# Optimization experiments

Measured on AMD Instinct MI355X. Metric: run time of the kernel, lower is better.

## Reference

```python
import jax, jax.numpy as jnp
import numpy as np

EPS = 1e-5  # torch BatchNorm2d default


def _conv1x1(x, w):
    # x: [n, cin, h, w], w: [cout, cin] (1x1 conv == per-pixel matmul)
    return jnp.einsum('nchw,oc->nohw', x, w)


def _bn(x, gamma, beta, mean, var):
    # inference-mode BatchNorm2d over channel dim
    scale = gamma * jax.lax.rsqrt(var + EPS)
    shift = beta - mean * scale
    return x * scale[None, :, None, None] + shift[None, :, None, None]


def setup_inputs() -> dict:
    key = jax.random.key(0)
    ks = jax.random.split(key, 24)
    n, c, h, w = 16, 256, 64, 64
    width, planes = c // 2, c
    inp = {
        'x': jax.random.normal(ks[0], (n, c, h, w), jnp.float32),
        'w_theta': jax.random.normal(ks[1], (width, c), jnp.float32) * 0.05,
        'w_phi': jax.random.normal(ks[2], (width, c), jnp.float32) * 0.05,
        'w_g': jax.random.normal(ks[3], (width, c), jnp.float32) * 0.05,
        'w_zeta': jax.random.normal(ks[4], (planes, width), jnp.float32) * 0.05,
    }
    for i, (name, dim) in enumerate([('bn1', width), ('bn2', width), ('bn3', width), ('bn4', planes)]):
        k = 5 + 4 * i
        inp[f'{name}_gamma'] = jax.random.uniform(ks[k], (dim,), jnp.float32, 0.5, 1.5)
        inp[f'{name}_beta'] = jax.random.normal(ks[k + 1], (dim,), jnp.float32) * 0.1
        inp[f'{name}_mean'] = jax.random.normal(ks[k + 2], (dim,), jnp.float32) * 0.1
        inp[f'{name}_var'] = jax.random.uniform(ks[k + 3], (dim,), jnp.float32, 0.5, 1.5)
    return inp


def reference(x, w_theta, w_phi, w_g, w_zeta,
              bn1_gamma, bn1_beta, bn1_mean, bn1_var,
              bn2_gamma, bn2_beta, bn2_mean, bn2_var,
              bn3_gamma, bn3_beta, bn3_mean, bn3_var,
              bn4_gamma, bn4_beta, bn4_mean, bn4_var):
    n, c, h, w = x.shape
    theta = jax.nn.relu(_bn(_conv1x1(x, w_theta), bn1_gamma, bn1_beta, bn1_mean, bn1_var))
    phi = jax.nn.relu(_bn(_conv1x1(x, w_phi), bn2_gamma, bn2_beta, bn2_mean, bn2_var))
    g = jax.nn.relu(_bn(_conv1x1(x, w_g), bn3_gamma, bn3_beta, bn3_mean, bn3_var))

    width = theta.shape[1]
    hw = h * w
    theta = theta.reshape(n, width, hw)  # [n, C', S]
    phi = phi.reshape(n, width, hw)      # [n, C', S]
    g = g.reshape(n, width, hw)          # [n, C', S]

    # (theta^T @ phi) @ g^T == theta^T @ (phi @ g^T): no softmax, so associativity
    # lets us contract over pixels first -> O(S*C'^2) instead of O(S^2*C').
    kv = jnp.einsum('ncs,nds->ncd', phi, g)      # [n, C', C']
    out = jnp.einsum('ncs,ncd->nsd', theta, kv)  # [n, S, C']

    # faithful to torch: reshape (not transpose) [n, S, C'] -> [n, C', h, w]
    out = out.reshape(n, width, h, w)
    out = _bn(_conv1x1(out, w_zeta), bn4_gamma, bn4_beta, bn4_mean, bn4_var)
    return jax.nn.relu(out + x)
```

## Files before the change

kernel.cpp:

```cpp
#include <hip/hip_runtime.h>

#define BN_EPS 1e-5f

typedef unsigned short u16;
typedef __bf16 bf16x8 __attribute__((ext_vector_type(8)));
typedef float floatx4 __attribute__((ext_vector_type(4)));
typedef u16 u16x4 __attribute__((ext_vector_type(4)));
typedef u16 u16x8 __attribute__((ext_vector_type(8)));

__device__ __forceinline__ u16 f2bf(float f) {
    union { float f; unsigned int u; } v; v.f = f;
    unsigned int r = (v.u + 0x7fffu + ((v.u >> 16) & 1u)) >> 16;
    return (u16)r;
}

__device__ __forceinline__ void gld16(const void* gsrc, void* ldst) {
    __builtin_amdgcn_global_load_lds(
        (const __attribute__((address_space(1))) unsigned int*)gsrc,
        (__attribute__((address_space(3))) unsigned int*)ldst, 16, 0, 0);
}

__device__ __forceinline__ int addsw(int seg, int s) {
    return (seg + (s & 7) + ((s >> 3) & 7)) & 7;
}

__global__ __launch_bounds__(256) void prep_kernel(
    const float* __restrict__ wt, const float* __restrict__ wp,
    const float* __restrict__ wg, const float* __restrict__ wz,
    const float* __restrict__ g1, const float* __restrict__ b1,
    const float* __restrict__ m1, const float* __restrict__ v1,
    const float* __restrict__ g2, const float* __restrict__ b2,
    const float* __restrict__ m2, const float* __restrict__ v2,
    const float* __restrict__ g3, const float* __restrict__ b3,
    const float* __restrict__ m3, const float* __restrict__ v3,
    const float* __restrict__ g4, const float* __restrict__ b4,
    const float* __restrict__ m4, const float* __restrict__ v4,
    u16* __restrict__ W1bf, float* __restrict__ shift1,
    u16* __restrict__ Wzbf, float* __restrict__ shift4)
{
    int id = blockIdx.x * 256 + threadIdx.x;
    if (id < 384 * 256) {
        int r = id >> 8, c = id & 255;
        int grp = r >> 7, ch = r & 127;
        const float* wsrc = grp == 0 ? wt : (grp == 1 ? wp : wg);
        const float* gg = grp == 0 ? g1 : (grp == 1 ? g2 : g3);
        const float* bb = grp == 0 ? b1 : (grp == 1 ? b2 : b3);
        const float* mm = grp == 0 ? m1 : (grp == 1 ? m2 : m3);
        const float* vv = grp == 0 ? v1 : (grp == 1 ? v2 : v3);
        float scale = gg[ch] * rsqrtf(vv[ch] + BN_EPS);
        W1bf[id] = f2bf(wsrc[ch * 256 + c] * scale);
        if (c == 0) shift1[r] = bb[ch] - mm[ch] * scale;
    }
    if (id < 256 * 128) {
        int o = id >> 7;
        float scale = g4[o] * rsqrtf(v4[o] + BN_EPS);
        Wzbf[id] = f2bf(wz[id] * scale);
        if ((id & 127) == 0) shift4[o] = b4[o] - m4[o] * scale;
    }
}

__global__ __launch_bounds__(256) void gemm1_kernel(
    const float* __restrict__ x, const u16* __restrict__ W1,
    const float* __restrict__ shift1,
    u16* __restrict__ theta_sm, u16* __restrict__ pg)
{
    const int st = blockIdx.x, mt = blockIdx.y, n = blockIdx.z;
    const int tid = threadIdx.x;
    const int w = tid >> 6, lane = tid & 63;
    const int quad = lane >> 4, l16 = lane & 15;

    __shared__ __align__(16) u16 ldsA[128 * 64];
    __shared__ __align__(16) u16 ldsB[128 * 64];

    floatx4 acc[2][8];
#pragma unroll
    for (int i = 0; i < 2; ++i)
#pragma unroll
        for (int j = 0; j < 8; ++j) acc[i][j] = floatx4{0.f, 0.f, 0.f, 0.f};

    const int s4 = tid & 31;
    const int cg = tid >> 5;
    const float* xbase = x + ((size_t)n * 256) * 4096 + st * 128;
    unsigned int* ldsBdw = (unsigned int*)ldsB;

    float4 xv0[4], xv1[4];
#pragma unroll
    for (int p = 0; p < 4; ++p) {
        int c0 = 2 * cg + 16 * p;
        xv0[p] = *((const float4*)(xbase + (size_t)c0 * 4096) + s4);
        xv1[p] = *((const float4*)(xbase + (size_t)(c0 + 1) * 4096) + s4);
    }

    for (int kc = 0; kc < 4; ++kc) {
#pragma unroll
        for (int p = 0; p < 4; ++p) {
            int cp = cg + 8 * p, slog = cp >> 2, dwin = cp & 3;
#pragma unroll
            for (int j = 0; j < 4; ++j) {
                int s = 4 * s4 + j;
                unsigned int pk = (unsigned int)f2bf(((const float*)&xv0[p])[j])
                                | ((unsigned int)f2bf(((const float*)&xv1[p])[j]) << 16);
                ldsBdw[s * 32 + addsw(slog, s) * 4 + dwin] = pk;
            }
        }
#pragma unroll
        for (int i = 0; i < 4; ++i) {
            int op = w * 4 + i;
            int r = op * 8 + (lane >> 3);
            int lseg = (lane & 7) ^ (r & 7);
            gld16(W1 + (size_t)(mt * 128 + r) * 256 + kc * 64 + lseg * 8,
                  ldsA + op * 512);
        }
        if (kc < 3) {
#pragma unroll
            for (int p = 0; p < 4; ++p) {
                int c0 = 2 * cg + 16 * p;
                xv0[p] = *((const float4*)(xbase + (size_t)((kc + 1) * 64 + c0) * 4096) + s4);
                xv1[p] = *((const float4*)(xbase + (size_t)((kc + 1) * 64 + c0 + 1) * 4096) + s4);
            }
        }
        __syncthreads();

#pragma unroll
        for (int kk = 0; kk < 2; ++kk) {
            bf16x8 a[2];
#pragma unroll
            for (int mi = 0; mi < 2; ++mi) {
                int r = w * 32 + mi * 16 + l16;
                int phys = (kk * 4 + quad) ^ (r & 7);
                a[mi] = *(const bf16x8*)(ldsA + r * 64 + phys * 8);
            }
#pragma unroll
            for (int ni = 0; ni < 8; ++ni) {
                int s = ni * 16 + l16;
                int phys = addsw(kk * 4 + quad, s);
                bf16x8 b = *(const bf16x8*)(ldsB + s * 64 + phys * 8);
#pragma unroll
                for (int mi = 0; mi < 2; ++mi)
                    acc[mi][ni] = __builtin_amdgcn_mfma_f32_16x16x32_bf16(
                        a[mi], b, acc[mi][ni], 0, 0, 0);
            }
        }
        __syncthreads();
    }

    if (mt == 0) {
#pragma unroll
        for (int mi = 0; mi < 2; ++mi) {
            int ocb = w * 32 + mi * 16 + quad * 4;
            float sh0 = shift1[ocb + 0], sh1 = shift1[ocb + 1];
            float sh2 = shift1[ocb + 2], sh3 = shift1[ocb + 3];
#pragma unroll
            for (int ni = 0; ni < 8; ++ni) {
                int s = st * 128 + ni * 16 + l16;
                float v0 = acc[mi][ni][0] + sh0, v1 = acc[mi][ni][1] + sh1;
                float v2 = acc[mi][ni][2] + sh2, v3 = acc[mi][ni][3] + sh3;
                u16x4 pk;
                pk[0] = f2bf(v0 > 0.f ? v0 : 0.f);
                pk[1] = f2bf(v1 > 0.f ? v1 : 0.f);
                pk[2] = f2bf(v2 > 0.f ? v2 : 0.f);
                pk[3] = f2bf(v3 > 0.f ? v3 : 0.f);
                *(u16x4*)(theta_sm + (size_t)n * 524288 + (size_t)s * 128 + ocb) = pk;
            }
        }
    } else {
#pragma unroll
        for (int mi = 0; mi < 2; ++mi)
#pragma unroll
            for (int r = 0; r < 4; ++r) {
                int oc = mt * 128 + w * 32 + mi * 16 + quad * 4 + r;
                int prow = (mt - 1) * 128 + w * 32 + mi * 16 + quad * 4 + r;
                float sh = shift1[oc];
#pragma unroll
                for (int ni = 0; ni < 8; ++ni) {
                    int s = st * 128 + ni * 16 + l16;
                    float val = acc[mi][ni][r] + sh;
                    val = val > 0.f ? val : 0.f;
                    pg[(size_t)n * 1048576 + (size_t)prow * 4096 + s] = f2bf(val);
                }
            }
    }
}

__global__ __launch_bounds__(512) void gemm2_kernel(
    const u16* __restrict__ pg, float* __restrict__ partials)
{
    const int kc = blockIdx.x, n = blockIdx.y;
    const int tid = threadIdx.x;
    const int w = tid >> 6, lane = tid & 63;
    const int quad = lane >> 4, l16 = lane & 15;

    __shared__ __align__(16) u16 ldsG[128 * 64];
    __shared__ __align__(16) u16 ldsP[128 * 64];

    floatx4 acc[2][4];
#pragma unroll
    for (int i = 0; i < 2; ++i)
#pragma unroll
        for (int j = 0; j < 4; ++j) acc[i][j] = floatx4{0.f, 0.f, 0.f, 0.f};

    const int d0 = (w >> 1) * 32, c0 = (w & 1) * 64;
    const u16* base = pg + (size_t)n * 1048576;

    for (int ch = 0; ch < 4; ++ch) {
        int s0 = kc * 256 + ch * 64;
#pragma unroll
        for (int i = 0; i < 2; ++i) {
            int op = w * 2 + i;
            int r = op * 8 + (lane >> 3);
            int lseg = (lane & 7) ^ (r & 7);
            gld16(base + (size_t)(128 + r) * 4096 + s0 + lseg * 8, ldsG + op * 512);
            gld16(base + (size_t)r * 4096 + s0 + lseg * 8, ldsP + op * 512);
        }
        __syncthreads();

#pragma unroll
        for (int kk = 0; kk < 2; ++kk) {
            bf16x8 a[2];
#pragma unroll
            for (int mi = 0; mi < 2; ++mi) {
                int r = d0 + mi * 16 + l16;
                int phys = (kk * 4 + quad) ^ (r & 7);
                a[mi] = *(const bf16x8*)(ldsG + r * 64 + phys * 8);
            }
#pragma unroll
            for (int ci = 0; ci < 4; ++ci) {
                int r = c0 + ci * 16 + l16;
                int phys = (kk * 4 + quad) ^ (r & 7);
                bf16x8 b = *(const bf16x8*)(ldsP + r * 64 + phys * 8);
#pragma unroll
                for (int mi = 0; mi < 2; ++mi)
                    acc[mi][ci] = __builtin_amdgcn_mfma_f32_16x16x32_bf16(
                        a[mi], b, acc[mi][ci], 0, 0, 0);
            }
        }
        __syncthreads();
    }

    float* outp = partials + (size_t)(n * 16 + kc) * 16384;
#pragma unroll
    for (int mi = 0; mi < 2; ++mi)
#pragma unroll
        for (int r = 0; r < 4; ++r) {
            int d = d0 + mi * 16 + quad * 4 + r;
#pragma unroll
            for (int ci = 0; ci < 4; ++ci)
                outp[d * 128 + c0 + ci * 16 + l16] = acc[mi][ci][r];
        }
}

__global__ __launch_bounds__(256) void kv_reduce_kernel(
    const float* __restrict__ partials, u16* __restrict__ kvT)
{
    int n = blockIdx.y;
    int f4 = blockIdx.x * 256 + threadIdx.x;
    const float4* p4 = (const float4*)partials;
    float4 s = {0.f, 0.f, 0.f, 0.f};
#pragma unroll
    for (int kc = 0; kc < 16; ++kc) {
        float4 v = p4[(size_t)(n * 16 + kc) * 4096 + f4];
        s.x += v.x; s.y += v.y; s.z += v.z; s.w += v.w;
    }
    u16x4 o; o[0] = f2bf(s.x); o[1] = f2bf(s.y); o[2] = f2bf(s.z); o[3] = f2bf(s.w);
    *(u16x4*)(kvT + (size_t)n * 16384 + f4 * 4) = o;
}

__global__ __launch_bounds__(256) void gemm3_kernel(
    const u16* __restrict__ theta_sm, const u16* __restrict__ kvT,
    u16* __restrict__ out_sd)
{
    const int st = blockIdx.x, n = blockIdx.y;
    const int tid = threadIdx.x;
    const int w = tid >> 6, lane = tid & 63;
    const int quad = lane >> 4, l16 = lane & 15;

    __shared__ __align__(16) u16 ldsT[128 * 64];
    __shared__ __align__(16) u16 ldsK[128 * 64];

    floatx4 acc[2][8];
#pragma unroll
    for (int i = 0; i < 2; ++i)
#pragma unroll
        for (int j = 0; j < 8; ++j) acc[i][j] = floatx4{0.f, 0.f, 0.f, 0.f};

    const u16* tbase = theta_sm + (size_t)n * 524288 + (size_t)st * 128 * 128;
    const u16* kbase = kvT + (size_t)n * 16384;

    for (int ch = 0; ch < 2; ++ch) {
#pragma unroll
        for (int i = 0; i < 4; ++i) {
            int op = w * 4 + i;
            int r = op * 8 + (lane >> 3);
            int lseg = (lane & 7) ^ (r & 7);
            gld16(tbase + (size_t)r * 128 + ch * 64 + lseg * 8, ldsT + op * 512);
            gld16(kbase + (size_t)r * 128 + ch * 64 + lseg * 8, ldsK + op * 512);
        }
        __syncthreads();

#pragma unroll
        for (int kk = 0; kk < 2; ++kk) {
            bf16x8 a[2];
#pragma unroll
            for (int mi = 0; mi < 2; ++mi) {
                int r = w * 32 + mi * 16 + l16;
                int phys = (kk * 4 + quad) ^ (r & 7);
                a[mi] = *(const bf16x8*)(ldsT + r * 64 + phys * 8);
            }
#pragma unroll
            for (int di = 0; di < 8; ++di) {
                int r = di * 16 + l16;
                int phys = (kk * 4 + quad) ^ (r & 7);
                bf16x8 b = *(const bf16x8*)(ldsK + r * 64 + phys * 8);
#pragma unroll
                for (int mi = 0; mi < 2; ++mi)
                    acc[mi][di] = __builtin_amdgcn_mfma_f32_16x16x32_bf16(
                        a[mi], b, acc[mi][di], 0, 0, 0);
            }
        }
        __syncthreads();
    }

#pragma unroll
    for (int mi = 0; mi < 2; ++mi)
#pragma unroll
        for (int r = 0; r < 4; ++r) {
            int s = st * 128 + w * 32 + mi * 16 + quad * 4 + r;
#pragma unroll
            for (int di = 0; di < 8; ++di)
                out_sd[(size_t)n * 524288 + (size_t)s * 128 + di * 16 + l16] =
                    f2bf(acc[mi][di][r]);
        }
}

__global__ __launch_bounds__(256) void gemm4_kernel(
    const u16* __restrict__ out_sd, const u16* __restrict__ Wz,
    const float* __restrict__ shift4, const float* __restrict__ x,
    float* __restrict__ out)
{
    const int st = blockIdx.x, ot = blockIdx.y, n = blockIdx.z;
    const int tid = threadIdx.x;
    const int w = tid >> 6, lane = tid & 63;
    const int quad = lane >> 4, l16 = lane & 15;

    __shared__ __align__(16) u16 ldsY[128 * 64];
    __shared__ __align__(16) u16 ldsW[128 * 64];

    floatx4 acc[2][8];
#pragma unroll
    for (int i = 0; i < 2; ++i)
#pragma unroll
        for (int j = 0; j < 8; ++j) acc[i][j] = floatx4{0.f, 0.f, 0.f, 0.f};

    const int sl = tid & 15;
    const int cg = tid >> 4;
    const u16* ybase = out_sd + (size_t)n * 524288 + st * 128;
    unsigned int* ldsYdw = (unsigned int*)ldsY;

    u16x8 yv0[2], yv1[2];
#pragma unroll
    for (int p = 0; p < 2; ++p) {
        int c0 = 2 * cg + 32 * p;
        yv0[p] = *(const u16x8*)(ybase + (size_t)c0 * 4096 + 8 * sl);
        yv1[p] = *(const u16x8*)(ybase + (size_t)(c0 + 1) * 4096 + 8 * sl);
    }

    for (int kc = 0; kc < 2; ++kc) {
#pragma unroll
        for (int p = 0; p < 2; ++p) {
            int cp = cg + 16 * p, slog = cp >> 2, dwin = cp & 3;
#pragma unroll
            for (int j = 0; j < 8; ++j) {
                int s = 8 * sl + j;
                unsigned int pk = (unsigned int)yv0[p][j] | ((unsigned int)yv1[p][j] << 16);
                ldsYdw[s * 32 + addsw(slog, s) * 4 + dwin] = pk;
            }
        }
#pragma unroll
        for (int i = 0; i < 4; ++i) {
            int op = w * 4 + i;
            int r = op * 8 + (lane >> 3);
            int lseg = (lane & 7) ^ (r & 7);
            gld16(Wz + (size_t)(ot * 128 + r) * 128 + kc * 64 + lseg * 8, ldsW + op * 512);
        }
        if (kc < 1) {
#pragma unroll
            for (int p = 0; p < 2; ++p) {
                int c0 = 2 * cg + 32 * p;
                yv0[p] = *(const u16x8*)(ybase + (size_t)(64 + c0) * 4096 + 8 * sl);
                yv1[p] = *(const u16x8*)(ybase + (size_t)(64 + c0 + 1) * 4096 + 8 * sl);
            }
        }
        __syncthreads();

#pragma unroll
        for (int kk = 0; kk < 2; ++kk) {
            bf16x8 a[2];
#pragma unroll
            for (int mi = 0; mi < 2; ++mi) {
                int r = w * 32 + mi * 16 + l16;
                int phys = (kk * 4 + quad) ^ (r & 7);
                a[mi] = *(const bf16x8*)(ldsW + r * 64 + phys * 8);
            }
#pragma unroll
            for (int ni = 0; ni < 8; ++ni) {
                int s = ni * 16 + l16;
                int phys = addsw(kk * 4 + quad, s);
                bf16x8 b = *(const bf16x8*)(ldsY + s * 64 + phys * 8);
#pragma unroll
                for (int mi = 0; mi < 2; ++mi)
                    acc[mi][ni] = __builtin_amdgcn_mfma_f32_16x16x32_bf16(
                        a[mi], b, acc[mi][ni], 0, 0, 0);
            }
        }
        __syncthreads();
    }

#pragma unroll
    for (int mi = 0; mi < 2; ++mi)
#pragma unroll
        for (int r = 0; r < 4; ++r) {
            int o = ot * 128 + w * 32 + mi * 16 + quad * 4 + r;
            float sh = shift4[o];
#pragma unroll
            for (int ni = 0; ni < 8; ++ni) {
                int s2 = st * 128 + ni * 16 + l16;
                size_t idx = ((size_t)n * 256 + o) * 4096 + s2;
                float val = acc[mi][ni][r] + sh + x[idx];
                out[idx] = val > 0.f ? val : 0.f;
            }
        }
}

extern "C" void kernel_launch(void* const* d_in, const int* in_sizes, int n_in,
                              void* d_out, int out_size, void* d_ws, size_t ws_size,
                              hipStream_t stream)
{
    const float* x  = (const float*)d_in[0];
    const float* wt = (const float*)d_in[1];
    const float* wp = (const float*)d_in[2];
    const float* wg = (const float*)d_in[3];
    const float* wz = (const float*)d_in[4];
    const float* bn[16];
    for (int i = 0; i < 16; ++i) bn[i] = (const float*)d_in[5 + i];

    char* ws = (char*)d_ws;
    u16*   W1bf     = (u16*)  (ws + 0);
    float* shift1   = (float*)(ws + 196608);
    u16*   Wzbf     = (u16*)  (ws + 198144);
    float* shift4   = (float*)(ws + 263680);
    u16*   theta_sm = (u16*)  (ws + 264704);
    u16*   pg       = (u16*)  (ws + 17041920);
    float* partials = (float*)(ws + 50596352);
    u16*   kvT      = (u16*)  (ws + 67373568);
    u16*   out_sd   = (u16*)  (ws + 67897856);
    float* out = (float*)d_out;

    prep_kernel<<<384, 256, 0, stream>>>(
        wt, wp, wg, wz,
        bn[0], bn[1], bn[2], bn[3],
        bn[4], bn[5], bn[6], bn[7],
        bn[8], bn[9], bn[10], bn[11],
        bn[12], bn[13], bn[14], bn[15],
        W1bf, shift1, Wzbf, shift4);

    gemm1_kernel<<<dim3(32, 3, 16), 256, 0, stream>>>(x, W1bf, shift1, theta_sm, pg);
    gemm2_kernel<<<dim3(16, 16), 512, 0, stream>>>(pg, partials);
    kv_reduce_kernel<<<dim3(16, 16), 256, 0, stream>>>(partials, kvT);
    gemm3_kernel<<<dim3(32, 16), 256, 0, stream>>>(theta_sm, kvT, out_sd);
    gemm4_kernel<<<dim3(32, 2, 16), 256, 0, stream>>>(out_sd, Wzbf, shift4, x, out);
}
```

Measured before the change: 219.8 us.

## Pre-transpose x to bf16 pixel-major and retile gemm2 with aliased workspace

Adds an xt_kernel that converts x to bf16 once and transposes it to pixel-major layout. gemm1 can then stream its B operand straight into LDS with direct global-to-LDS loads instead of redoing fp32 loads, conversion and scattered LDS writes in each of the 3 M-tile blocks. gemm2 moves to 256 threads with a larger per-wave tile and 32 split-K chunks, and the workspace buffers are re-laid out to alias each other. The cost is an extra kernel launch, an extra round trip through a bf16 copy of x, and more partials for kv_reduce to sum.

```diff
diff --git a/kernel.cpp b/kernel.cpp
--- a/kernel.cpp
+++ b/kernel.cpp
@@ -18,10 +18,6 @@
     __builtin_amdgcn_global_load_lds(
         (const __attribute__((address_space(1))) unsigned int*)gsrc,
         (__attribute__((address_space(3))) unsigned int*)ldst, 16, 0, 0);
-}
-
-__device__ __forceinline__ int addsw(int seg, int s) {
-    return (seg + (s & 7) + ((s >> 3) & 7)) & 7;
 }
 
 __global__ __launch_bounds__(256) void prep_kernel(
@@ -59,8 +55,41 @@
     }
 }
 
+__global__ __launch_bounds__(256) void xt_kernel(
+    const float* __restrict__ x, u16* __restrict__ xt)
+{
+    const int stile = blockIdx.x, n = blockIdx.y;
+    const int t = threadIdx.x;
+    __shared__ __align__(16) u16 lds[64 * 256];
+
+    const float* xb = x + (size_t)n * 1048576 + stile * 64;
+    const int crow0 = t >> 4, sf4 = t & 15;
+#pragma unroll
+    for (int i = 0; i < 16; ++i) {
+        int c = crow0 + 16 * i;
+        float4 v = *((const float4*)(xb + (size_t)c * 4096) + sf4);
+        int cseg = c >> 3, cin = c & 7;
+#pragma unroll
+        for (int j = 0; j < 4; ++j) {
+            int s = sf4 * 4 + j;
+            int csw = (cseg & ~7) | ((cseg ^ (s >> 2)) & 7);
+            lds[s * 256 + csw * 8 + cin] = f2bf(((const float*)&v)[j]);
+        }
+    }
+    __syncthreads();
+
+    const int so = t >> 2, c4 = t & 3;
+    u16* ob = xt + (size_t)n * 1048576 + (size_t)(stile * 64 + so) * 256;
+#pragma unroll
+    for (int i = 0; i < 8; ++i) {
+        int cseg = c4 + 4 * i;
+        int csw = (cseg & ~7) | ((cseg ^ (so >> 2)) & 7);
+        *(u16x8*)(ob + cseg * 8) = *(const u16x8*)(lds + so * 256 + csw * 8);
+    }
+}
+
 __global__ __launch_bounds__(256) void gemm1_kernel(
-    const float* __restrict__ x, const u16* __restrict__ W1,
+    const u16* __restrict__ xt, const u16* __restrict__ W1,
     const float* __restrict__ shift1,
     u16* __restrict__ theta_sm, u16* __restrict__ pg)
 {
@@ -78,31 +107,9 @@
 #pragma unroll
         for (int j = 0; j < 8; ++j) acc[i][j] = floatx4{0.f, 0.f, 0.f, 0.f};
 
-    const int s4 = tid & 31;
-    const int cg = tid >> 5;
-    const float* xbase = x + ((size_t)n * 256) * 4096 + st * 128;
-    unsigned int* ldsBdw = (unsigned int*)ldsB;
-
-    float4 xv0[4], xv1[4];
-#pragma unroll
-    for (int p = 0; p < 4; ++p) {
-        int c0 = 2 * cg + 16 * p;
-        xv0[p] = *((const float4*)(xbase + (size_t)c0 * 4096) + s4);
-        xv1[p] = *((const float4*)(xbase + (size_t)(c0 + 1) * 4096) + s4);
-    }
+    const u16* xb = xt + (size_t)n * 1048576 + (size_t)st * 128 * 256;
 
     for (int kc = 0; kc < 4; ++kc) {
-#pragma unroll
-        for (int p = 0; p < 4; ++p) {
-            int cp = cg + 8 * p, slog = cp >> 2, dwin = cp & 3;
-#pragma unroll
-            for (int j = 0; j < 4; ++j) {
-                int s = 4 * s4 + j;
-                unsigned int pk = (unsigned int)f2bf(((const float*)&xv0[p])[j])
-                                | ((unsigned int)f2bf(((const float*)&xv1[p])[j]) << 16);
-                ldsBdw[s * 32 + addsw(slog, s) * 4 + dwin] = pk;
-            }
-        }
 #pragma unroll
         for (int i = 0; i < 4; ++i) {
             int op = w * 4 + i;
@@ -110,14 +117,8 @@
             int lseg = (lane & 7) ^ (r & 7);
             gld16(W1 + (size_t)(mt * 128 + r) * 256 + kc * 64 + lseg * 8,
                   ldsA + op * 512);
-        }
-        if (kc < 3) {
-#pragma unroll
-            for (int p = 0; p < 4; ++p) {
-                int c0 = 2 * cg + 16 * p;
-                xv0[p] = *((const float4*)(xbase + (size_t)((kc + 1) * 64 + c0) * 4096) + s4);
-                xv1[p] = *((const float4*)(xbase + (size_t)((kc + 1) * 64 + c0 + 1) * 4096) + s4);
-            }
+            gld16(xb + (size_t)r * 256 + kc * 64 + lseg * 8,
+                  ldsB + op * 512);
         }
         __syncthreads();
 
@@ -133,7 +134,7 @@
 #pragma unroll
             for (int ni = 0; ni < 8; ++ni) {
                 int s = ni * 16 + l16;
-                int phys = addsw(kk * 4 + quad, s);
+                int phys = (kk * 4 + quad) ^ (s & 7);
                 bf16x8 b = *(const bf16x8*)(ldsB + s * 64 + phys * 8);
 #pragma unroll
                 for (int mi = 0; mi < 2; ++mi)
@@ -182,7 +183,7 @@
     }
 }
 
-__global__ __launch_bounds__(512) void gemm2_kernel(
+__global__ __launch_bounds__(256) void gemm2_kernel(
     const u16* __restrict__ pg, float* __restrict__ partials)
 {
     const int kc = blockIdx.x, n = blockIdx.y;
@@ -193,20 +194,19 @@
     __shared__ __align__(16) u16 ldsG[128 * 64];
     __shared__ __align__(16) u16 ldsP[128 * 64];
 
-    floatx4 acc[2][4];
+    floatx4 acc[2][8];
 #pragma unroll
     for (int i = 0; i < 2; ++i)
 #pragma unroll
-        for (int j = 0; j < 4; ++j) acc[i][j] = floatx4{0.f, 0.f, 0.f, 0.f};
-
-    const int d0 = (w >> 1) * 32, c0 = (w & 1) * 64;
+        for (int j = 0; j < 8; ++j) acc[i][j] = floatx4{0.f, 0.f, 0.f, 0.f};
+
     const u16* base = pg + (size_t)n * 1048576;
 
-    for (int ch = 0; ch < 4; ++ch) {
-        int s0 = kc * 256 + ch * 64;
-#pragma unroll
-        for (int i = 0; i < 2; ++i) {
-            int op = w * 2 + i;
+    for (int ch = 0; ch < 2; ++ch) {
+        int s0 = kc * 128 + ch * 64;
+#pragma unroll
+        for (int i = 0; i < 4; ++i) {
+            int op = w * 4 + i;
             int r = op * 8 + (lane >> 3);
             int lseg = (lane & 7) ^ (r & 7);
             gld16(base + (size_t)(128 + r) * 4096 + s0 + lseg * 8, ldsG + op * 512);
@@ -219,13 +219,13 @@
             bf16x8 a[2];
 #pragma unroll
             for (int mi = 0; mi < 2; ++mi) {
-                int r = d0 + mi * 16 + l16;
+                int r = w * 32 + mi * 16 + l16;
                 int phys = (kk * 4 + quad) ^ (r & 7);
                 a[mi] = *(const bf16x8*)(ldsG + r * 64 + phys * 8);
             }
 #pragma unroll
-            for (int ci = 0; ci < 4; ++ci) {
-                int r = c0 + ci * 16 + l16;
+            for (int ci = 0; ci < 8; ++ci) {
+                int r = ci * 16 + l16;
                 int phys = (kk * 4 + quad) ^ (r & 7);
                 bf16x8 b = *(const bf16x8*)(ldsP + r * 64 + phys * 8);
 #pragma unroll
@@ -237,15 +237,15 @@
         __syncthreads();
     }
 
-    float* outp = partials + (size_t)(n * 16 + kc) * 16384;
+    float* outp = partials + (size_t)(n * 32 + kc) * 16384;
 #pragma unroll
     for (int mi = 0; mi < 2; ++mi)
 #pragma unroll
         for (int r = 0; r < 4; ++r) {
-            int d = d0 + mi * 16 + quad * 4 + r;
-#pragma unroll
-            for (int ci = 0; ci < 4; ++ci)
-                outp[d * 128 + c0 + ci * 16 + l16] = acc[mi][ci][r];
+            int d = w * 32 + mi * 16 + quad * 4 + r;
+#pragma unroll
+            for (int ci = 0; ci < 8; ++ci)
+                outp[d * 128 + ci * 16 + l16] = acc[mi][ci][r];
         }
 }
 
@@ -257,8 +257,8 @@
     const float4* p4 = (const float4*)partials;
     float4 s = {0.f, 0.f, 0.f, 0.f};
 #pragma unroll
-    for (int kc = 0; kc < 16; ++kc) {
-        float4 v = p4[(size_t)(n * 16 + kc) * 4096 + f4];
+    for (int kc = 0; kc < 32; ++kc) {
+        float4 v = p4[(size_t)(n * 32 + kc) * 4096 + f4];
         s.x += v.x; s.y += v.y; s.z += v.z; s.w += v.w;
     }
     u16x4 o; o[0] = f2bf(s.x); o[1] = f2bf(s.y); o[2] = f2bf(s.z); o[3] = f2bf(s.w);
@@ -330,6 +330,10 @@
                 out_sd[(size_t)n * 524288 + (size_t)s * 128 + di * 16 + l16] =
                     f2bf(acc[mi][di][r]);
         }
+}
+
+__device__ __forceinline__ int addsw(int seg, int s) {
+    return (seg + (s & 7) + ((s >> 3) & 7)) & 7;
 }
 
 __global__ __launch_bounds__(256) void gemm4_kernel(
@@ -448,11 +452,12 @@
     float* shift1   = (float*)(ws + 196608);
     u16*   Wzbf     = (u16*)  (ws + 198144);
     float* shift4   = (float*)(ws + 263680);
-    u16*   theta_sm = (u16*)  (ws + 264704);
-    u16*   pg       = (u16*)  (ws + 17041920);
-    float* partials = (float*)(ws + 50596352);
-    u16*   kvT      = (u16*)  (ws + 67373568);
-    u16*   out_sd   = (u16*)  (ws + 67897856);
+    u16*   xt       = (u16*)  (ws + 264704);
+    float* partials = (float*)(ws + 264704);
+    u16*   theta_sm = (u16*)  (ws + 33819136);
+    u16*   pg       = (u16*)  (ws + 50596352);
+    u16*   out_sd   = (u16*)  (ws + 50596352);
+    u16*   kvT      = (u16*)  (ws + 84150784 - 524288);
     float* out = (float*)d_out;
 
     prep_kernel<<<384, 256, 0, stream>>>(
@@ -463,8 +468,9 @@
         bn[12], bn[13], bn[14], bn[15],
         W1bf, shift1, Wzbf, shift4);
 
-    gemm1_kernel<<<dim3(32, 3, 16), 256, 0, stream>>>(x, W1bf, shift1, theta_sm, pg);
-    gemm2_kernel<<<dim3(16, 16), 512, 0, stream>>>(pg, partials);
+    xt_kernel<<<dim3(64, 16), 256, 0, stream>>>(x, xt);
+    gemm1_kernel<<<dim3(32, 3, 16), 256, 0, stream>>>(xt, W1bf, shift1, theta_sm, pg);
+    gemm2_kernel<<<dim3(32, 16), 256, 0, stream>>>(pg, partials);
     kv_reduce_kernel<<<dim3(16, 16), 256, 0, stream>>>(partials, kvT);
     gemm3_kernel<<<dim3(32, 16), 256, 0, stream>>>(theta_sm, kvT, out_sd);
     gemm4_kernel<<<dim3(32, 2, 16), 256, 0, stream>>>(out_sd, Wzbf, shift4, x, out);
```

Result: slower. 234.1 us (+6.5%).
